# Kernel tuning notes

Measured on AMD Instinct MI355X. Metric: run time of the kernel, lower is better.

The kernel has to match this reference:

```python
import jax, jax.numpy as jnp
import numpy as np

EPS_NORM = 1e-6
EPS_Q = 1e-5


def rmsnorm(x, g):
    ms = jnp.mean(x * x, axis=-1, keepdims=True)
    return x * jax.lax.rsqrt(ms + EPS_NORM) * g


def bitlinear(x, w, g):
    # RMSNorm -> absmax int8 activation quant -> absmean ternary weight quant -> matmul -> rescale
    xn = rmsnorm(x, g)
    x_scale = jnp.maximum(jnp.max(jnp.abs(xn), axis=-1, keepdims=True), EPS_Q)
    xq = jnp.clip(jnp.round(xn * 127.0 / x_scale), -128.0, 127.0)  # STE irrelevant in fwd
    w_scale = jnp.maximum(jnp.mean(jnp.abs(w)), EPS_Q)
    wq = jnp.clip(jnp.round(w / w_scale), -1.0, 1.0)
    out = jnp.einsum('btd,od->bto', xq, wq)
    return out * (w_scale * x_scale / 127.0)


def rotate_half(x):
    d = x.shape[-1] // 2
    return jnp.concatenate([-x[..., d:], x[..., :d]], axis=-1)


def apply_rope(x, cos, sin):
    # x: [B, H, T, D]; cos/sin: [T, D]
    return x * cos[None, None] + rotate_half(x) * sin[None, None]


def setup_inputs() -> dict:
    key = jax.random.key(0)
    ks = jax.random.split(key, 12)
    B, T, D, H, KV = 2, 2048, 2048, 32, 8
    hd = D // H
    bound = 1.0 / np.sqrt(D)  # ~ kaiming_uniform fan_in
    inp = {
        'x': jax.random.normal(ks[0], (B, T, D), jnp.float32),
        'cos': jax.random.uniform(ks[1], (T, hd), jnp.float32),
        'sin': jax.random.uniform(ks[2], (T, hd), jnp.float32),
        'wq': jax.random.uniform(ks[3], (H * hd, D), jnp.float32, -bound, bound),
        'wk': jax.random.uniform(ks[4], (KV * hd, D), jnp.float32, -bound, bound),
        'wv': jax.random.uniform(ks[5], (KV * hd, D), jnp.float32, -bound, bound),
        'wo': jax.random.uniform(ks[6], (D, H * hd), jnp.float32, -bound, bound),
        'gq': jnp.ones((D,), jnp.float32),
        'gk': jnp.ones((D,), jnp.float32),
        'gv': jnp.ones((D,), jnp.float32),
        'go': jnp.ones((H * hd,), jnp.float32),
    }
    return inp


def reference(x, cos, sin, wq, wk, wv, wo, gq, gk, gv, go):
    B, T, D = x.shape
    H, KV = 32, 8
    hd = D // H
    n_rep = H // KV

    q = bitlinear(x, wq, gq).reshape(B, T, H, hd).transpose(0, 2, 1, 3)   # [B,H,T,hd]
    k = bitlinear(x, wk, gk).reshape(B, T, KV, hd).transpose(0, 2, 1, 3)  # [B,KV,T,hd]
    v = bitlinear(x, wv, gv).reshape(B, T, KV, hd).transpose(0, 2, 1, 3)

    q = apply_rope(q, cos, sin)
    k = apply_rope(k, cos, sin)

    # GQA repeat_interleave on head dim
    k = jnp.repeat(k, n_rep, axis=1)  # [B,H,T,hd]
    v = jnp.repeat(v, n_rep, axis=1)

    scale = 1.0 / np.sqrt(hd)
    scores = jnp.einsum('bhqd,bhkd->bhqk', q, k) * scale
    causal = jnp.tril(jnp.ones((T, T), bool))
    scores = jnp.where(causal, scores, jnp.finfo(scores.dtype).min)
    attn = jax.nn.softmax(scores, axis=-1)
    out = jnp.einsum('bhqk,bhkd->bhqd', attn, v)
    out = out.transpose(0, 2, 1, 3).reshape(B, T, H * hd)
    return bitlinear(out, wo, go)
```

## Files before the change

kernel.cpp:

```cpp
#include <hip/hip_runtime.h>
#include <stdint.h>

constexpr int B   = 2;
constexpr int T   = 2048;
constexpr int D   = 2048;
constexpr int H   = 32;
constexpr int KVH = 8;
constexpr int HD  = 64;
constexpr int R   = B * T;
constexpr int OKV = KVH * HD;

using bf16x8 = __attribute__((ext_vector_type(8))) __bf16;
using f32x4  = __attribute__((ext_vector_type(4))) float;
using i32x4  = __attribute__((ext_vector_type(4))) int;

__device__ inline float fast_exp2(float x) {
#if __has_builtin(__builtin_amdgcn_exp2f)
    return __builtin_amdgcn_exp2f(x);
#else
    return exp2f(x);
#endif
}

__device__ inline uint16_t f2bf(float f) {
    uint32_t u = __float_as_uint(f);
    u += 0x7fff + ((u >> 16) & 1);
    return (uint16_t)(u >> 16);
}

__device__ inline uint32_t pack_bf16(float a, float b) {
#if __has_builtin(__builtin_amdgcn_cvt_pk_bf16_f32)
    union { __attribute__((ext_vector_type(2))) __bf16 v; uint32_t u; } r;
    r.v = __builtin_amdgcn_cvt_pk_bf16_f32(a, b);
    return r.u;
#else
    return (uint32_t)f2bf(a) | ((uint32_t)f2bf(b) << 16);
#endif
}

__device__ inline void async16(const void* g, void* l) {
    __builtin_amdgcn_global_load_lds((const __attribute__((address_space(1))) unsigned int*)g,
                                     (__attribute__((address_space(3))) unsigned int*)l,
                                     16, 0, 0);
}

__global__ void absmean4_kernel(const float* __restrict__ w0, const float* __restrict__ w1,
                                const float* __restrict__ w2, const float* __restrict__ w3,
                                double* __restrict__ sums) {
    __shared__ float red[256];
    const float* ws[4] = {w0, w1, w2, w3};
    const int ns[4] = {D * D, OKV * D, OKV * D, D * D};
    int wi = blockIdx.y;
    const float* w = ws[wi];
    int n = ns[wi];
    int tid = threadIdx.x;
    float s = 0.f;
    for (int i = blockIdx.x * 256 + tid; i < n; i += gridDim.x * 256)
        s += fabsf(w[i]);
    red[tid] = s;
    __syncthreads();
    for (int st = 128; st > 0; st >>= 1) {
        if (tid < st) red[tid] += red[tid + st];
        __syncthreads();
    }
    if (tid == 0) atomicAdd(&sums[wi], (double)red[0]);
}

__global__ void quantw4_kernel(const float* __restrict__ w0, const float* __restrict__ w1,
                               const float* __restrict__ w2, const float* __restrict__ w3,
                               int8_t* __restrict__ o0, int8_t* __restrict__ o1,
                               int8_t* __restrict__ o2, int8_t* __restrict__ o3,
                               const double* __restrict__ sums) {
    const float* ws[4] = {w0, w1, w2, w3};
    int8_t* os[4] = {o0, o1, o2, o3};
    const int ns[4] = {D * D, OKV * D, OKV * D, D * D};
    int wi = blockIdx.y;
    const float* w = ws[wi];
    int8_t* o = os[wi];
    int n = ns[wi];
    float wsc = fmaxf((float)(sums[wi] / (double)n), 1e-5f);
    for (int i = blockIdx.x * 256 + threadIdx.x; i < n; i += gridDim.x * 256) {
        float q = rintf(w[i] / wsc);
        q = fminf(fmaxf(q, -1.f), 1.f);
        o[i] = (int8_t)q;
    }
}

__global__ __launch_bounds__(256) void rmsq3_kernel(const float* __restrict__ X,
        const float* __restrict__ g0, const float* __restrict__ g1, const float* __restrict__ g2,
        int8_t* __restrict__ o0, int8_t* __restrict__ o1, int8_t* __restrict__ o2,
        float* __restrict__ s0, float* __restrict__ s1, float* __restrict__ s2) {
    __shared__ float red[256];
    int row = blockIdx.x, tid = threadIdx.x;
    const float* xr = X + (size_t)row * D;
    float xv[8];
    float ss = 0.f;
#pragma unroll
    for (int i = 0; i < 8; i++) { xv[i] = xr[tid + 256 * i]; ss += xv[i] * xv[i]; }
    red[tid] = ss;
    __syncthreads();
    for (int st = 128; st > 0; st >>= 1) {
        if (tid < st) red[tid] += red[tid + st];
        __syncthreads();
    }
    float rstd = 1.0f / sqrtf(red[0] / (float)D + 1e-6f);

    const float* gs[3] = {g0, g1, g2};
    int8_t* os[3] = {o0, o1, o2};
    float* sc[3] = {s0, s1, s2};
#pragma unroll
    for (int v = 0; v < 3; v++) {
        float xn[8];
        float amax = 0.f;
#pragma unroll
        for (int i = 0; i < 8; i++) {
            xn[i] = xv[i] * rstd * gs[v][tid + 256 * i];
            amax = fmaxf(amax, fabsf(xn[i]));
        }
        __syncthreads();
        red[tid] = amax;
        __syncthreads();
        for (int st = 128; st > 0; st >>= 1) {
            if (tid < st) red[tid] = fmaxf(red[tid], red[tid + st]);
            __syncthreads();
        }
        float xsv = fmaxf(red[0], 1e-5f);
        float q127 = 127.0f / xsv;
#pragma unroll
        for (int i = 0; i < 8; i++) {
            float q = rintf(xn[i] * q127);
            q = fminf(fmaxf(q, -128.f), 127.f);
            os[v][(size_t)row * D + tid + 256 * i] = (int8_t)q;
        }
        if (tid == 0) sc[v][row] = xsv;
    }
}

__global__ void rmsq_kernel(const float* __restrict__ X, const float* __restrict__ g,
                            int8_t* __restrict__ Xq, float* __restrict__ xs_out) {
    __shared__ float red[256];
    int row = blockIdx.x;
    int tid = threadIdx.x;
    const float* xr = X + (size_t)row * D;

    float ss = 0.f;
    for (int i = tid; i < D; i += 256) { float v = xr[i]; ss += v * v; }
    red[tid] = ss;
    __syncthreads();
    for (int st = 128; st > 0; st >>= 1) {
        if (tid < st) red[tid] += red[tid + st];
        __syncthreads();
    }
    float ms = red[0] / (float)D;
    float rstd = 1.0f / sqrtf(ms + 1e-6f);
    __syncthreads();

    float amax = 0.f;
    for (int i = tid; i < D; i += 256) {
        float xn = xr[i] * rstd * g[i];
        amax = fmaxf(amax, fabsf(xn));
    }
    red[tid] = amax;
    __syncthreads();
    for (int st = 128; st > 0; st >>= 1) {
        if (tid < st) red[tid] = fmaxf(red[tid], red[tid + st]);
        __syncthreads();
    }
    float xs = fmaxf(red[0], 1e-5f);

    for (int i = tid; i < D; i += 256) {
        float xn = xr[i] * rstd * g[i];
        float q = rintf(xn * 127.0f / xs);
        q = fminf(fmaxf(q, -128.f), 127.f);
        Xq[(size_t)row * D + i] = (int8_t)q;
    }
    if (tid == 0) xs_out[row] = xs;
}

template<int BN, int MODE>
__global__ __launch_bounds__(256) void gemm_i8_mfma(const int8_t* __restrict__ Xq,
                                                    const int8_t* __restrict__ W8,
                                                    void* __restrict__ outp,
                                                    const float* __restrict__ xs,
                                                    const double* __restrict__ wsum, int wi,
                                                    int nw, int O,
                                                    const float* __restrict__ cs,
                                                    const float* __restrict__ sn) {
    constexpr int NT = BN / 16;
    __shared__ __align__(16) uint8_t As[128 * 128];
    __shared__ __align__(16) uint8_t Bs[BN * 128];

    const int tid  = threadIdx.x;
    const int lane = tid & 63;
    const int wv   = tid >> 6;
    const int n    = lane & 15, quad = lane >> 4;
    const int row0 = blockIdx.y * 128;
    const int col0 = blockIdx.x * BN;

    i32x4 acc[2][NT] = {};

    for (int k0 = 0; k0 < D; k0 += 128) {
        __syncthreads();
#pragma unroll
        for (int j = 0; j < 4; j++) {
            int p = wv * 256 + j * 64 + lane;
            int r = p >> 3, s = p & 7;
            int c = s ^ (r & 7);
            async16(Xq + (size_t)(row0 + r) * D + k0 + c * 16,
                    &As[(size_t)(wv * 256 + j * 64) * 16]);
        }
#pragma unroll
        for (int j = 0; j < BN / 32; j++) {
            int p = wv * (BN * 2) + j * 64 + lane;
            int r = p >> 3, s = p & 7;
            int c = s ^ (r & 7);
            async16(W8 + (size_t)(col0 + r) * D + k0 + c * 16,
                    &Bs[(size_t)(wv * (BN * 2) + j * 64) * 16]);
        }
        __syncthreads();
#pragma unroll
        for (int t = 0; t < 2; t++) {
            i32x4 af[2], bfr[NT];
#pragma unroll
            for (int mt = 0; mt < 2; mt++) {
                int r = wv * 32 + mt * 16 + n;
                af[mt] = *(const i32x4*)&As[r * 128 + (((t * 4 + quad) ^ (r & 7)) * 16)];
            }
#pragma unroll
            for (int nt = 0; nt < NT; nt++) {
                int r = nt * 16 + n;
                bfr[nt] = *(const i32x4*)&Bs[r * 128 + (((t * 4 + quad) ^ (r & 7)) * 16)];
            }
#pragma unroll
            for (int mt = 0; mt < 2; mt++)
#pragma unroll
                for (int nt = 0; nt < NT; nt++)
                    acc[mt][nt] = __builtin_amdgcn_mfma_i32_16x16x64_i8(af[mt], bfr[nt], acc[mt][nt], 0, 0, 0);
        }
    }
    float w = fmaxf((float)(wsum[wi] / (double)nw), 1e-5f);
#pragma unroll
    for (int mt = 0; mt < 2; mt++) {
#pragma unroll
        for (int r2 = 0; r2 < 4; r2++) {
            int row = row0 + wv * 32 + mt * 16 + quad * 4 + r2;
            float f = w * xs[row] * (1.0f / 127.0f);
            if (MODE == 0) {
                float* out = (float*)outp;
#pragma unroll
                for (int nt = 0; nt < NT; nt++)
                    out[(size_t)row * O + col0 + nt * 16 + n] = (float)acc[mt][nt][r2] * f;
            } else {
                uint16_t* out = (uint16_t*)outp;
                int t = row & (T - 1);
#pragma unroll
                for (int nt = 0; nt < NT; nt++) {
                    if ((nt & 3) >= 2) continue;
                    int i = (nt * 16 + n) & 63;
                    float a  = (float)acc[mt][nt][r2] * f;
                    float bb = (float)acc[mt][nt + 2][r2] * f;
                    float c0 = cs[t * HD + i],      s0 = sn[t * HD + i];
                    float c1 = cs[t * HD + i + 32], s1 = sn[t * HD + i + 32];
                    out[(size_t)row * O + col0 + nt * 16 + n]       = f2bf(a * c0 - bb * s0);
                    out[(size_t)row * O + col0 + (nt + 2) * 16 + n] = f2bf(bb * c1 + a * s1);
                }
            }
        }
    }
}

__global__ __launch_bounds__(256) void vtrans_kernel(const float* __restrict__ vb,
                                                     uint16_t* __restrict__ vt) {
    __shared__ float tile[64][65];
    int t0 = blockIdx.x * 64;
    int hb = blockIdx.y;
    int b = hb >> 3, kvh = hb & 7;
    int tid = threadIdx.x;
    int r = tid >> 2, cg = (tid & 3) * 16;
#pragma unroll
    for (int j = 0; j < 4; j++) {
        float4 v4 = *(const float4*)(vb + (size_t)(b * T + t0 + r) * OKV + kvh * HD + cg + j * 4);
        tile[r][cg + j * 4 + 0] = v4.x;
        tile[r][cg + j * 4 + 1] = v4.y;
        tile[r][cg + j * 4 + 2] = v4.z;
        tile[r][cg + j * 4 + 3] = v4.w;
    }
    __syncthreads();
    int d = tid >> 2, tg = (tid & 3) * 16;
    uint16_t pk[16];
#pragma unroll
    for (int j = 0; j < 16; j++) pk[j] = f2bf(tile[tg + j][d]);
    *(uint4*)(vt + ((size_t)hb * 64 + d) * T + t0 + tg)     = *(uint4*)&pk[0];
    *(uint4*)(vt + ((size_t)hb * 64 + d) * T + t0 + tg + 8) = *(uint4*)&pk[8];
}

__global__ __launch_bounds__(256, 2) void attn_mfma_kernel(const uint16_t* __restrict__ qh,
                                                           const uint16_t* __restrict__ kh,
                                                           const uint16_t* __restrict__ vt,
                                                           float* __restrict__ out) {
    __shared__ __align__(16) uint16_t KsB[2][64 * 64];
    __shared__ __align__(16) uint16_t VtB[2][64 * 64];
    __shared__ __align__(16) uint16_t Pw[4][16 * 72];

    const int tid  = threadIdx.x;
    const int lane = tid & 63;
    const int wv   = tid >> 6;
    const int p = blockIdx.x, h = blockIdx.y, b = blockIdx.z;
    const int kvh = h >> 2;
    const int n = lane & 15, quad = lane >> 4;
    const float SC = 0.125f * 1.44269504089f;

    union { bf16x8 v; uint16_t u[8]; } onesf;
#pragma unroll
    for (int j = 0; j < 8; j++) onesf.u[j] = 0x3F80;

    int q_lo[4];
#pragma unroll
    for (int i = 0; i < 4; i++)
        q_lo[i] = ((i < 2) ? p : (15 - p)) * 128 + wv * 32 + (i & 1) * 16;

    bf16x8 qf[4][2];
#pragma unroll
    for (int i = 0; i < 4; i++) {
        const uint16_t* qp = qh + (size_t)(b * T + q_lo[i] + n) * D + h * HD + quad * 8;
        qf[i][0] = *(const bf16x8*)(qp);
        qf[i][1] = *(const bf16x8*)(qp + 32);
    }

    f32x4 o[4][4] = {};
    f32x4 lacc[4] = {};
    float m[4];
#pragma unroll
    for (int i = 0; i < 4; i++) m[i] = -INFINITY;

    const uint16_t* kbase = kh + (size_t)b * T * OKV + kvh * HD;
    const uint16_t* vbase = vt + (size_t)(b * KVH + kvh) * 64 * T;

    const int nch = 32 - 2 * p;

#pragma unroll
    for (int j = 0; j < 2; j++) {
        int pp = wv * 128 + j * 64 + lane;
        int r = pp >> 3, sl = pp & 7;
        int c = sl ^ (r & 7);
        async16(kbase + (size_t)r * OKV + c * 8, &KsB[0][(wv * 128 + j * 64) * 8]);
        async16(vbase + (size_t)r * T + c * 8,   &VtB[0][(wv * 128 + j * 64) * 8]);
    }
    __syncthreads();

    for (int ch = 0; ch < nch; ch++) {
        const int cur = ch & 1;
        if (ch + 1 < nch) {
            const int t1 = (ch + 1) * 64;
#pragma unroll
            for (int j = 0; j < 2; j++) {
                int pp = wv * 128 + j * 64 + lane;
                int r = pp >> 3, sl = pp & 7;
                int c = sl ^ (r & 7);
                async16(kbase + (size_t)(t1 + r) * OKV + c * 8, &KsB[cur ^ 1][(wv * 128 + j * 64) * 8]);
                async16(vbase + (size_t)r * T + t1 + c * 8,     &VtB[cur ^ 1][(wv * 128 + j * 64) * 8]);
            }
        }
        const int t0 = ch * 64;

        bf16x8 kf[2][4], vf[2][4];
#pragma unroll
        for (int ks = 0; ks < 2; ks++)
#pragma unroll
            for (int mt = 0; mt < 4; mt++) {
                int r = mt * 16 + n;
                int cc = (((ks * 4 + quad) ^ (n & 7)) * 8);
                kf[ks][mt] = *(const bf16x8*)&KsB[cur][r * 64 + cc];
                vf[ks][mt] = *(const bf16x8*)&VtB[cur][r * 64 + cc];
            }

#pragma unroll
        for (int i = 0; i < 4; i++) {
            if (t0 > q_lo[i] + 15) continue;
            f32x4 sv[4] = {};
#pragma unroll
            for (int ks = 0; ks < 2; ks++)
#pragma unroll
                for (int mt = 0; mt < 4; mt++)
                    sv[mt] = __builtin_amdgcn_mfma_f32_16x16x32_bf16(kf[ks][mt], qf[i][ks], sv[mt], 0, 0, 0);

            const int qg = q_lo[i] + n;
            const bool diag = (t0 + 63 > q_lo[i]);
            float mloc = -INFINITY;
#pragma unroll
            for (int mt = 0; mt < 4; mt++)
#pragma unroll
                for (int r2 = 0; r2 < 4; r2++) {
                    float x = sv[mt][r2];
                    if (diag) {
                        int kg = t0 + mt * 16 + quad * 4 + r2;
                        x = (kg > qg) ? -INFINITY : x;
                        sv[mt][r2] = x;
                    }
                    mloc = fmaxf(mloc, x);
                }
            mloc = fmaxf(mloc, __shfl_xor(mloc, 16));
            mloc = fmaxf(mloc, __shfl_xor(mloc, 32));
            bool upd = (mloc > m[i]);
            if (__ballot(upd)) {
                float mnew = fmaxf(m[i], mloc);
                float corr = upd ? fast_exp2((m[i] - mnew) * SC) : 1.0f;
                m[i] = mnew;
#pragma unroll
                for (int mt = 0; mt < 4; mt++)
#pragma unroll
                    for (int r2 = 0; r2 < 4; r2++) o[i][mt][r2] *= corr;
                lacc[i][0] *= corr;
            }
            float msc = m[i] * SC;
#pragma unroll
            for (int mt = 0; mt < 4; mt++) {
                float pv[4];
#pragma unroll
                for (int r2 = 0; r2 < 4; r2++)
                    pv[r2] = fast_exp2(__builtin_fmaf(sv[mt][r2], SC, -msc));
                uint2 w2;
                w2.x = pack_bf16(pv[0], pv[1]);
                w2.y = pack_bf16(pv[2], pv[3]);
                *(uint2*)&Pw[wv][n * 72 + mt * 16 + quad * 4] = w2;
            }
#pragma unroll
            for (int ks = 0; ks < 2; ks++) {
                bf16x8 pf = *(const bf16x8*)&Pw[wv][n * 72 + ks * 32 + quad * 8];
#pragma unroll
                for (int mt = 0; mt < 4; mt++)
                    o[i][mt] = __builtin_amdgcn_mfma_f32_16x16x32_bf16(vf[ks][mt], pf, o[i][mt], 0, 0, 0);
                lacc[i] = __builtin_amdgcn_mfma_f32_16x16x32_bf16(onesf.v, pf, lacc[i], 0, 0, 0);
            }
        }
        __syncthreads();
    }

#pragma unroll
    for (int i = 0; i < 4; i++) {
        int qg = q_lo[i] + n;
        float inv = 1.0f / lacc[i][0];
#pragma unroll
        for (int mt = 0; mt < 4; mt++) {
            f32x4 ov;
#pragma unroll
            for (int r2 = 0; r2 < 4; r2++) ov[r2] = o[i][mt][r2] * inv;
            *(f32x4*)(out + (size_t)(b * T + qg) * D + h * HD + mt * 16 + quad * 4) = ov;
        }
    }
}

extern "C" void kernel_launch(void* const* d_in, const int* in_sizes, int n_in,
                              void* d_out, int out_size, void* d_ws, size_t ws_size,
                              hipStream_t stream) {
    const float* x   = (const float*)d_in[0];
    const float* cs  = (const float*)d_in[1];
    const float* sn  = (const float*)d_in[2];
    const float* wq  = (const float*)d_in[3];
    const float* wk  = (const float*)d_in[4];
    const float* wv  = (const float*)d_in[5];
    const float* wo  = (const float*)d_in[6];
    const float* gq  = (const float*)d_in[7];
    const float* gk  = (const float*)d_in[8];
    const float* gv  = (const float*)d_in[9];
    const float* go  = (const float*)d_in[10];
    float* out = (float*)d_out;

    uint8_t* w = (uint8_t*)d_ws;
    double* wsum  = (double*)w;
    float* xs     = (float*)(w + 256);
    size_t off = 256 + 4 * (size_t)R * 4;
    int8_t* Wq8 = (int8_t*)(w + off); off += (size_t)D * D;
    int8_t* Wk8 = (int8_t*)(w + off); off += (size_t)OKV * D;
    int8_t* Wv8 = (int8_t*)(w + off); off += (size_t)OKV * D;
    int8_t* Wo8 = (int8_t*)(w + off); off += (size_t)D * D;
    int8_t* Xq_q = (int8_t*)(w + off); off += (size_t)R * D;
    int8_t* Xq_k = (int8_t*)(w + off); off += (size_t)R * D;
    int8_t* Xq_v = (int8_t*)(w + off); off += (size_t)R * D;
    float* ab = (float*)(w + off); off += (size_t)R * D * 4;
    float* vb = (float*)(w + off); off += (size_t)R * OKV * 4;
    uint16_t* qhb = (uint16_t*)(w + off); off += (size_t)R * D * 2;
    uint16_t* khb = (uint16_t*)Xq_v;
    uint16_t* vtb = (uint16_t*)Xq_k;
    int8_t*   Aq8 = Xq_q;

    (void)hipMemsetAsync(wsum, 0, 64, stream);

    absmean4_kernel<<<dim3(256, 4), 256, 0, stream>>>(wq, wk, wv, wo, wsum);
    quantw4_kernel<<<dim3(1024, 4), 256, 0, stream>>>(wq, wk, wv, wo, Wq8, Wk8, Wv8, Wo8, wsum);

    rmsq3_kernel<<<R, 256, 0, stream>>>(x, gq, gk, gv, Xq_q, Xq_k, Xq_v,
                                        xs + 0 * R, xs + 1 * R, xs + 2 * R);

    gemm_i8_mfma<128, 1><<<dim3(D / 128, R / 128), 256, 0, stream>>>(
        Xq_q, Wq8, qhb, xs + 0 * R, wsum, 0, D * D, D, cs, sn);
    gemm_i8_mfma<64, 0><<<dim3(OKV / 64, R / 128), 256, 0, stream>>>(
        Xq_v, Wv8, vb, xs + 2 * R, wsum, 2, OKV * D, OKV, cs, sn);
    gemm_i8_mfma<64, 1><<<dim3(OKV / 64, R / 128), 256, 0, stream>>>(
        Xq_k, Wk8, khb, xs + 1 * R, wsum, 1, OKV * D, OKV, cs, sn);

    vtrans_kernel<<<dim3(T / 64, B * KVH), 256, 0, stream>>>(vb, vtb);

    attn_mfma_kernel<<<dim3(8, H, B), 256, 0, stream>>>(qhb, khb, vtb, ab);

    rmsq_kernel<<<R, 256, 0, stream>>>(ab, go, Aq8, xs + 3 * R);
    gemm_i8_mfma<128, 0><<<dim3(D / 128, R / 128), 256, 0, stream>>>(
        Aq8, Wo8, out, xs + 3 * R, wsum, 3, D * D, D, cs, sn);
}
```

Measured before the change: 386.1 us.

## Split attention across eight waves, defer softmax rescale, prioritize MFMA issue

The attention block grows from 256 to 512 threads. Each wave now owns two 16-row query tiles instead of four, which halves per-wave registers and raises the number of waves that can hide latency. The online-softmax rescale is skipped unless the running max grows by a margin, which cuts the correction multiplies but lets exponentials grow up to about 2^8 before normalization. MFMA sections are wrapped in s_setprio to favor matrix issue across waves. The risks are added barrier cost with more waves sharing each K/V tile, and some loss of precision in the bf16 probabilities.

```diff
diff --git a/kernel.cpp b/kernel.cpp
--- a/kernel.cpp
+++ b/kernel.cpp
@@ -294,13 +294,13 @@
     *(uint4*)(vt + ((size_t)hb * 64 + d) * T + t0 + tg + 8) = *(uint4*)&pk[8];
 }
 
-__global__ __launch_bounds__(256, 2) void attn_mfma_kernel(const uint16_t* __restrict__ qh,
+__global__ __launch_bounds__(512, 4) void attn_mfma_kernel(const uint16_t* __restrict__ qh,
                                                            const uint16_t* __restrict__ kh,
                                                            const uint16_t* __restrict__ vt,
                                                            float* __restrict__ out) {
     __shared__ __align__(16) uint16_t KsB[2][64 * 64];
     __shared__ __align__(16) uint16_t VtB[2][64 * 64];
-    __shared__ __align__(16) uint16_t Pw[4][16 * 72];
+    __shared__ __align__(16) uint16_t Pw[8][16 * 72];
 
     const int tid  = threadIdx.x;
     const int lane = tid & 63;
@@ -309,42 +309,36 @@
     const int kvh = h >> 2;
     const int n = lane & 15, quad = lane >> 4;
     const float SC = 0.125f * 1.44269504089f;
+    const float DEFER = 44.3614f;
 
     union { bf16x8 v; uint16_t u[8]; } onesf;
 #pragma unroll
     for (int j = 0; j < 8; j++) onesf.u[j] = 0x3F80;
 
-    int q_lo[4];
-#pragma unroll
-    for (int i = 0; i < 4; i++)
-        q_lo[i] = ((i < 2) ? p : (15 - p)) * 128 + wv * 32 + (i & 1) * 16;
-
-    bf16x8 qf[4][2];
-#pragma unroll
-    for (int i = 0; i < 4; i++) {
+    int q_lo[2] = { p * 128 + wv * 16, (15 - p) * 128 + wv * 16 };
+
+    bf16x8 qf[2][2];
+#pragma unroll
+    for (int i = 0; i < 2; i++) {
         const uint16_t* qp = qh + (size_t)(b * T + q_lo[i] + n) * D + h * HD + quad * 8;
         qf[i][0] = *(const bf16x8*)(qp);
         qf[i][1] = *(const bf16x8*)(qp + 32);
     }
 
-    f32x4 o[4][4] = {};
-    f32x4 lacc[4] = {};
-    float m[4];
-#pragma unroll
-    for (int i = 0; i < 4; i++) m[i] = -INFINITY;
+    f32x4 o[2][4] = {};
+    f32x4 lacc[2] = {};
+    float m[2] = { -INFINITY, -INFINITY };
 
     const uint16_t* kbase = kh + (size_t)b * T * OKV + kvh * HD;
     const uint16_t* vbase = vt + (size_t)(b * KVH + kvh) * 64 * T;
 
     const int nch = 32 - 2 * p;
 
-#pragma unroll
-    for (int j = 0; j < 2; j++) {
-        int pp = wv * 128 + j * 64 + lane;
-        int r = pp >> 3, sl = pp & 7;
+    {
+        int r = tid >> 3, sl = tid & 7;
         int c = sl ^ (r & 7);
-        async16(kbase + (size_t)r * OKV + c * 8, &KsB[0][(wv * 128 + j * 64) * 8]);
-        async16(vbase + (size_t)r * T + c * 8,   &VtB[0][(wv * 128 + j * 64) * 8]);
+        async16(kbase + (size_t)r * OKV + c * 8, &KsB[0][wv * 512]);
+        async16(vbase + (size_t)r * T + c * 8,   &VtB[0][wv * 512]);
     }
     __syncthreads();
 
@@ -352,14 +346,10 @@
         const int cur = ch & 1;
         if (ch + 1 < nch) {
             const int t1 = (ch + 1) * 64;
-#pragma unroll
-            for (int j = 0; j < 2; j++) {
-                int pp = wv * 128 + j * 64 + lane;
-                int r = pp >> 3, sl = pp & 7;
-                int c = sl ^ (r & 7);
-                async16(kbase + (size_t)(t1 + r) * OKV + c * 8, &KsB[cur ^ 1][(wv * 128 + j * 64) * 8]);
-                async16(vbase + (size_t)r * T + t1 + c * 8,     &VtB[cur ^ 1][(wv * 128 + j * 64) * 8]);
-            }
+            int r = tid >> 3, sl = tid & 7;
+            int c = sl ^ (r & 7);
+            async16(kbase + (size_t)(t1 + r) * OKV + c * 8, &KsB[cur ^ 1][wv * 512]);
+            async16(vbase + (size_t)r * T + t1 + c * 8,     &VtB[cur ^ 1][wv * 512]);
         }
         const int t0 = ch * 64;
 
@@ -375,14 +365,16 @@
             }
 
 #pragma unroll
-        for (int i = 0; i < 4; i++) {
+        for (int i = 0; i < 2; i++) {
             if (t0 > q_lo[i] + 15) continue;
             f32x4 sv[4] = {};
+            __builtin_amdgcn_s_setprio(1);
 #pragma unroll
             for (int ks = 0; ks < 2; ks++)
 #pragma unroll
                 for (int mt = 0; mt < 4; mt++)
                     sv[mt] = __builtin_amdgcn_mfma_f32_16x16x32_bf16(kf[ks][mt], qf[i][ks], sv[mt], 0, 0, 0);
+            __builtin_amdgcn_s_setprio(0);
 
             const int qg = q_lo[i] + n;
             const bool diag = (t0 + 63 > q_lo[i]);
@@ -401,10 +393,10 @@
                 }
             mloc = fmaxf(mloc, __shfl_xor(mloc, 16));
             mloc = fmaxf(mloc, __shfl_xor(mloc, 32));
-            bool upd = (mloc > m[i]);
+            bool upd = (mloc > m[i] + DEFER);
             if (__ballot(upd)) {
                 float mnew = fmaxf(m[i], mloc);
-                float corr = upd ? fast_exp2((m[i] - mnew) * SC) : 1.0f;
+                float corr = fast_exp2((m[i] - mnew) * SC);
                 m[i] = mnew;
 #pragma unroll
                 for (int mt = 0; mt < 4; mt++)
@@ -424,6 +416,7 @@
                 w2.y = pack_bf16(pv[2], pv[3]);
                 *(uint2*)&Pw[wv][n * 72 + mt * 16 + quad * 4] = w2;
             }
+            __builtin_amdgcn_s_setprio(1);
 #pragma unroll
             for (int ks = 0; ks < 2; ks++) {
                 bf16x8 pf = *(const bf16x8*)&Pw[wv][n * 72 + ks * 32 + quad * 8];
@@ -432,12 +425,13 @@
                     o[i][mt] = __builtin_amdgcn_mfma_f32_16x16x32_bf16(vf[ks][mt], pf, o[i][mt], 0, 0, 0);
                 lacc[i] = __builtin_amdgcn_mfma_f32_16x16x32_bf16(onesf.v, pf, lacc[i], 0, 0, 0);
             }
-        }
-        __syncthreads();
-    }
-
-#pragma unroll
-    for (int i = 0; i < 4; i++) {
+            __builtin_amdgcn_s_setprio(0);
+        }
+        __syncthreads();
+    }
+
+#pragma unroll
+    for (int i = 0; i < 2; i++) {
         int qg = q_lo[i] + n;
         float inv = 1.0f / lacc[i][0];
 #pragma unroll
@@ -501,7 +495,7 @@
 
     vtrans_kernel<<<dim3(T / 64, B * KVH), 256, 0, stream>>>(vb, vtb);
 
-    attn_mfma_kernel<<<dim3(8, H, B), 256, 0, stream>>>(qhb, khb, vtb, ab);
+    attn_mfma_kernel<<<dim3(8, H, B), 512, 0, stream>>>(qhb, khb, vtb, ab);
 
     rmsq_kernel<<<R, 256, 0, stream>>>(ab, go, Aq8, xs + 3 * R);
     gemm_i8_mfma<128, 0><<<dim3(D / 128, R / 128), 256, 0, stream>>>(
```

Result: slower. 595.3 us (+54.2%).
